# Performance work log

Hardware: AMD Instinct MI355X
Metric: run time of the kernel (lower is better)

Reference implementation:

```python
import jax, jax.numpy as jnp
import numpy as np

INPUT_SIZE = 512
HIDDEN_SIZE = 1024
SEQ_LEN = 512
BATCH = 64


def _xavier(key, shape):
    fan_out, fan_in = shape
    limit = float(np.sqrt(6.0 / (fan_in + fan_out)))
    return jax.random.uniform(key, shape, jnp.float32, -limit, limit)


def setup_inputs() -> dict:
    key = jax.random.key(0)
    ks = jax.random.split(key, 10)
    return {
        "x_seq": jax.random.normal(ks[0], (SEQ_LEN, BATCH, INPUT_SIZE), jnp.float32),
        "h": jax.random.normal(ks[1], (BATCH, HIDDEN_SIZE), jnp.float32),
        "U_c": _xavier(ks[2], (HIDDEN_SIZE, INPUT_SIZE)),
        "w_c": jax.random.normal(ks[3], (HIDDEN_SIZE,), jnp.float32),
        "b_c": jax.random.normal(ks[4], (HIDDEN_SIZE,), jnp.float32),
        "U_a": _xavier(ks[5], (HIDDEN_SIZE, INPUT_SIZE)),
        "w_a": jax.random.normal(ks[6], (HIDDEN_SIZE,), jnp.float32),
        "b_a": jax.random.normal(ks[7], (HIDDEN_SIZE,), jnp.float32),
        "U_h": _xavier(ks[8], (HIDDEN_SIZE, INPUT_SIZE)),
        "b_h": jax.random.normal(ks[9], (HIDDEN_SIZE,), jnp.float32),
    }


def reference(x_seq, h, U_c, w_c, b_c, U_a, w_a, b_a, U_h, b_h):
    # Precompute all input projections in one big batched GEMM each:
    # (S, B, I) @ (I, H) -> (S, B, H)
    xc = jnp.einsum("sbi,hi->sbh", x_seq, U_c) + b_c
    xa = jnp.einsum("sbi,hi->sbh", x_seq, U_a) + b_a
    xh = jnp.einsum("sbi,hi->sbh", x_seq, U_h) + b_h

    def step(h, proj):
        pc, pa, ph = proj
        c = jax.nn.sigmoid(pc + w_c * h)
        a = 1.0 + jnp.tanh(pa + w_a * h)
        h_new = c * h + (1.0 - c) * jnp.tanh(ph + a * h)
        return h_new, h_new

    hn, y_seq = jax.lax.scan(step, h, (xc, xa, xh))
    return y_seq, hn
```

## Files before the change

kernel.cpp:

```cpp
#include <hip/hip_runtime.h>
#include <hip/hip_bf16.h>
#include <stdint.h>

#define SEQLEN 512
#define NBATCH 64
#define KDIM   512
#define HDIM   1024
#define MTOT   (SEQLEN * NBATCH)
#define NTOT   (3 * HDIM)
#define STRIDE (NBATCH * HDIM)

typedef __attribute__((ext_vector_type(4)))  float f32x4;
typedef __attribute__((ext_vector_type(16))) float f32x16;
typedef _Float16 f16x8 __attribute__((ext_vector_type(8)));

__global__ __launch_bounds__(256) void cvt_x(const float* __restrict__ x,
                                             _Float16* __restrict__ xh,
                                             _Float16* __restrict__ xl) {
    int i = blockIdx.x * 256 + threadIdx.x;
    const float4* s = (const float4*)(x + (size_t)i * 8);
    float4 a = s[0], b = s[1];
    float v[8] = {a.x, a.y, a.z, a.w, b.x, b.y, b.z, b.w};
    f16x8 hi, lo;
#pragma unroll
    for (int j = 0; j < 8; ++j) {
        _Float16 h = (_Float16)v[j];
        hi[j] = h;
        lo[j] = (_Float16)(v[j] - (float)h);
    }
    *(f16x8*)(xh + (size_t)i * 8) = hi;
    *(f16x8*)(xl + (size_t)i * 8) = lo;
}

__global__ __launch_bounds__(256) void cvt_u(const float* __restrict__ Uc,
                                             const float* __restrict__ Ua,
                                             const float* __restrict__ Uh,
                                             _Float16* __restrict__ uh,
                                             _Float16* __restrict__ ul) {
    int i = blockIdx.x * 256 + threadIdx.x;
    int n = i >> 6;
    int kb = (i & 63) * 8;
    const float* src = (n < HDIM) ? (Uc + (size_t)n * KDIM)
                     : (n < 2 * HDIM) ? (Ua + (size_t)(n - HDIM) * KDIM)
                     : (Uh + (size_t)(n - 2 * HDIM) * KDIM);
    const float4* s = (const float4*)(src + kb);
    float4 a = s[0], b = s[1];
    float v[8] = {a.x, a.y, a.z, a.w, b.x, b.y, b.z, b.w};
    f16x8 hi, lo;
#pragma unroll
    for (int j = 0; j < 8; ++j) {
        _Float16 h = (_Float16)v[j];
        hi[j] = h;
        lo[j] = (_Float16)(v[j] - (float)h);
    }
    *(f16x8*)(uh + (size_t)n * KDIM + kb) = hi;
    *(f16x8*)(ul + (size_t)n * KDIM + kb) = lo;
}

#define BM 256
#define BN 256
#define BK 32
#define NT_N (NTOT / BN)
#define GRID ((MTOT / BM) * NT_N)
#define KT_N (KDIM / BK)

__device__ __forceinline__ void gload16(const _Float16* g, _Float16* l) {
    __builtin_amdgcn_global_load_lds((const __attribute__((address_space(1))) void*)g,
                                     (__attribute__((address_space(3))) void*)l,
                                     16, 0, 0);
}

__device__ __forceinline__ f32x16 mfma32(f16x8 a, f16x8 b, f32x16 c) {
    return __builtin_amdgcn_mfma_f32_32x32x16_f16(a, b, c, 0, 0, 0);
}

__global__ __launch_bounds__(512, 2) void gemm_f16x2(const _Float16* __restrict__ Ah,
                                                     const _Float16* __restrict__ Al,
                                                     const _Float16* __restrict__ Bh,
                                                     const _Float16* __restrict__ Bl,
                                                     float* __restrict__ pc,
                                                     float* __restrict__ pa,
                                                     float* __restrict__ ph) {
    __shared__ _Float16 lds[2][4][BM * BK];

    int bid  = blockIdx.x;
    int bm   = bid / NT_N;
    int bn   = bid % NT_N;
    int tid  = threadIdx.x;
    int lane = tid & 63;
    int wave = tid >> 6;
    int wr   = wave >> 2;
    int wc   = wave & 3;

    size_t row_off = (size_t)(tid >> 2) * KDIM
                   + (size_t)(((tid & 3) ^ ((tid >> 3) & 3)) * 8);
    const _Float16* gAh = Ah + (size_t)bm * BM * KDIM + row_off;
    const _Float16* gAl = Al + (size_t)bm * BM * KDIM + row_off;
    const _Float16* gBh = Bh + (size_t)bn * BN * KDIM + row_off;
    const _Float16* gBl = Bl + (size_t)bn * BN * KDIM + row_off;
    const size_t HPAN = (size_t)128 * KDIM;
    int t8 = tid * 8;

#define SPAIR(buf, plane, gp, kt) do { int _g = (kt) * BK;                     \
    gload16((gp) + _g,        &lds[buf][plane][t8]);                           \
    gload16((gp) + HPAN + _g, &lds[buf][plane][t8 + 4096]); } while (0)

    f32x16 acc[4][2];
#pragma unroll
    for (int i = 0; i < 4; ++i)
#pragma unroll
        for (int j = 0; j < 2; ++j)
#pragma unroll
            for (int r = 0; r < 16; ++r)
                acc[i][j][r] = 0.f;

    int rr = lane & 31;
    int kg = lane >> 5;
    int kx = (lane >> 1) & 3;

    f16x8 a_[4][2], b_[2][2];

#define READ_A(ks) _Pragma("unroll")                                           \
    for (int i = 0; i < 4; ++i) {                                              \
        int row = wr * 128 + i * 32 + rr;                                      \
        int ko = ((((ks) * 2 + kg) ^ kx) * 8);                                 \
        a_[i][0] = *(const f16x8*)(&lds[cur][0][row * BK + ko]);               \
        a_[i][1] = *(const f16x8*)(&lds[cur][1][row * BK + ko]);               \
    }
#define READ_B(ks) _Pragma("unroll")                                           \
    for (int j = 0; j < 2; ++j) {                                              \
        int row = wc * 64 + j * 32 + rr;                                       \
        int ko = ((((ks) * 2 + kg) ^ kx) * 8);                                 \
        b_[j][0] = *(const f16x8*)(&lds[cur][2][row * BK + ko]);               \
        b_[j][1] = *(const f16x8*)(&lds[cur][3][row * BK + ko]);               \
    }
#define MFMA_STEP() _Pragma("unroll")                                          \
    for (int i = 0; i < 4; ++i) _Pragma("unroll")                              \
        for (int j = 0; j < 2; ++j) {                                          \
            f32x16 c = acc[i][j];                                              \
            c = mfma32(a_[i][0], b_[j][1], c);                      \
            c = mfma32(a_[i][1], b_[j][0], c);                      \
            c = mfma32(a_[i][0], b_[j][0], c);                      \
            acc[i][j] = c;                                                     \
        }

    SPAIR(0, 0, gAh, 0); SPAIR(0, 1, gAl, 0);
    SPAIR(0, 2, gBh, 0); SPAIR(0, 3, gBl, 0);

    for (int kt = 0; kt < KT_N; ++kt) {
        int cur = kt & 1, nxt = 1 - cur;
        bool pre = (kt < KT_N - 1);
        __builtin_amdgcn_sched_barrier(0);
        asm volatile("s_waitcnt vmcnt(0)" ::: "memory");
        __builtin_amdgcn_s_barrier();
        __builtin_amdgcn_sched_barrier(0);

        READ_B(0);
        READ_A(0);
        if (pre) { SPAIR(nxt, 0, gAh, kt + 1); SPAIR(nxt, 1, gAl, kt + 1); }
        __builtin_amdgcn_s_setprio(1);
        MFMA_STEP();
        __builtin_amdgcn_s_setprio(0);
        READ_A(1);
        READ_B(1);
        if (pre) { SPAIR(nxt, 2, gBh, kt + 1); SPAIR(nxt, 3, gBl, kt + 1); }
        __builtin_amdgcn_s_setprio(1);
        MFMA_STEP();
        __builtin_amdgcn_s_setprio(0);
    }

    int n0 = bn * BN;
    float* outp; int nb;
    if (n0 < HDIM)            { outp = pc; nb = n0; }
    else if (n0 < 2 * HDIM)   { outp = pa; nb = n0 - HDIM; }
    else                      { outp = ph; nb = n0 - 2 * HDIM; }

#pragma unroll
    for (int i = 0; i < 4; ++i)
#pragma unroll
        for (int j = 0; j < 2; ++j) {
            int mbase = bm * BM + wr * 128 + i * 32 + 4 * kg;
            int nn = nb + wc * 64 + j * 32 + rr;
#pragma unroll
            for (int t = 0; t < 4; ++t)
#pragma unroll
                for (int q = 0; q < 4; ++q)
                    outp[(size_t)(mbase + q + 8 * t) * HDIM + nn] = acc[i][j][t * 4 + q];
        }
#undef SPAIR
#undef READ_A
#undef READ_B
#undef MFMA_STEP
}

__device__ __forceinline__ float fsigmoid(float z) {
    float e = __expf(-z);
    return __builtin_amdgcn_rcpf(1.0f + e);
}
__device__ __forceinline__ float ftanh(float x) {
    float ax = fminf(fabsf(x), 10.0f);
    float e  = __expf(-2.0f * ax);
    float t  = (1.0f - e) * __builtin_amdgcn_rcpf(1.0f + e);
    return copysignf(t, x);
}

__global__ __launch_bounds__(256) void recur(const float* __restrict__ pc_a,
                                             const float* __restrict__ pa_a,
                                             float* out,
                                             const float* __restrict__ h0,
                                             const float* __restrict__ wc_,
                                             const float* __restrict__ bc_,
                                             const float* __restrict__ wa_,
                                             const float* __restrict__ ba_,
                                             const float* __restrict__ bh_) {
    int idx = blockIdx.x * 256 + threadIdx.x;
    int j = idx & (HDIM - 1);
    float h  = h0[idx];
    float wc = wc_[j], bc = bc_[j];
    float wa = wa_[j], ba = ba_[j];
    float bh = bh_[j];

#define PF 32
    float pc[PF], pa[PF], ph[PF];
#pragma unroll
    for (int u = 0; u < PF; ++u) {
        pc[u] = pc_a[(size_t)u * STRIDE + idx];
        pa[u] = pa_a[(size_t)u * STRIDE + idx];
        ph[u] = out [(size_t)u * STRIDE + idx];
    }

    for (int sb = 0; sb < SEQLEN; sb += PF) {
#pragma unroll
        for (int u = 0; u < PF; ++u) {
            int s = sb + u;
            float vc = pc[u], va = pa[u], vh = ph[u];
            int sp = s + PF; sp = (sp < SEQLEN) ? sp : (SEQLEN - 1);
            pc[u] = pc_a[(size_t)sp * STRIDE + idx];
            pa[u] = pa_a[(size_t)sp * STRIDE + idx];
            ph[u] = out [(size_t)sp * STRIDE + idx];

            float zc = (vc + bc) + wc * h;
            float za = (va + ba) + wa * h;
            float c  = fsigmoid(zc);
            float a  = 1.0f + ftanh(za);
            float ht = ftanh((vh + bh) + a * h);
            h = c * h + (1.0f - c) * ht;
            out[(size_t)s * STRIDE + idx] = h;
        }
    }
    out[(size_t)SEQLEN * STRIDE + idx] = h;
}

extern "C" void kernel_launch(void* const* d_in, const int* in_sizes, int n_in,
                              void* d_out, int out_size, void* d_ws, size_t ws_size,
                              hipStream_t stream) {
    const float* x_seq = (const float*)d_in[0];
    const float* h0    = (const float*)d_in[1];
    const float* U_c   = (const float*)d_in[2];
    const float* w_c   = (const float*)d_in[3];
    const float* b_c   = (const float*)d_in[4];
    const float* U_a   = (const float*)d_in[5];
    const float* w_a   = (const float*)d_in[6];
    const float* b_a   = (const float*)d_in[7];
    const float* U_h   = (const float*)d_in[8];
    const float* b_h   = (const float*)d_in[9];
    float* out = (float*)d_out;

    char* ws = (char*)d_ws;
    const size_t MB = 1024 * 1024;
    float*    ws_pc = (float*)ws;
    float*    ws_pa = (float*)(ws + 128 * MB);
    _Float16* x_hi  = (_Float16*)(ws + 256 * MB);
    _Float16* x_lo  = (_Float16*)(ws + 288 * MB);
    _Float16* u_hi  = (_Float16*)(ws + 320 * MB);
    _Float16* u_lo  = (_Float16*)(ws + 323 * MB);

    cvt_x<<<dim3(MTOT * KDIM / 8 / 256), dim3(256), 0, stream>>>(x_seq, x_hi, x_lo);
    cvt_u<<<dim3(NTOT * KDIM / 8 / 256), dim3(256), 0, stream>>>(U_c, U_a, U_h, u_hi, u_lo);
    gemm_f16x2<<<dim3(GRID), dim3(512), 0, stream>>>(
        x_hi, x_lo, u_hi, u_lo, ws_pc, ws_pa, out);
    recur<<<dim3(STRIDE / 256), dim3(256), 0, stream>>>(ws_pc, ws_pa, out, h0,
                                                        w_c, b_c, w_a, b_a, b_h);
}
```

Before: 494.2 us.

## Merge conversion kernels, deepen LDS swizzle, shrink recurrence prefetch, use libm activations

```diff
diff --git a/kernel.cpp b/kernel.cpp
--- a/kernel.cpp
+++ b/kernel.cpp
@@ -14,11 +14,35 @@
 typedef __attribute__((ext_vector_type(16))) float f32x16;
 typedef _Float16 f16x8 __attribute__((ext_vector_type(8)));
 
-__global__ __launch_bounds__(256) void cvt_x(const float* __restrict__ x,
-                                             _Float16* __restrict__ xh,
-                                             _Float16* __restrict__ xl) {
+#define XTHREADS (MTOT * KDIM / 8)
+#define UTHREADS (NTOT * KDIM / 8)
+__global__ __launch_bounds__(256) void cvt_all(const float* __restrict__ x,
+                                               const float* __restrict__ Uc,
+                                               const float* __restrict__ Ua,
+                                               const float* __restrict__ Uh,
+                                               _Float16* __restrict__ xh,
+                                               _Float16* __restrict__ xl,
+                                               _Float16* __restrict__ uh,
+                                               _Float16* __restrict__ ul) {
     int i = blockIdx.x * 256 + threadIdx.x;
-    const float4* s = (const float4*)(x + (size_t)i * 8);
+    const float* src;
+    _Float16 *dh, *dl;
+    size_t off;
+    if (i < XTHREADS) {
+        src = x + (size_t)i * 8;
+        off = (size_t)i * 8;
+        dh = xh; dl = xl;
+    } else {
+        int u = i - XTHREADS;
+        int n = u >> 6;
+        int kb = (u & 63) * 8;
+        src = ((n < HDIM) ? (Uc + (size_t)n * KDIM)
+             : (n < 2 * HDIM) ? (Ua + (size_t)(n - HDIM) * KDIM)
+             : (Uh + (size_t)(n - 2 * HDIM) * KDIM)) + kb;
+        off = (size_t)n * KDIM + kb;
+        dh = uh; dl = ul;
+    }
+    const float4* s = (const float4*)src;
     float4 a = s[0], b = s[1];
     float v[8] = {a.x, a.y, a.z, a.w, b.x, b.y, b.z, b.w};
     f16x8 hi, lo;
@@ -28,33 +52,8 @@
         hi[j] = h;
         lo[j] = (_Float16)(v[j] - (float)h);
     }
-    *(f16x8*)(xh + (size_t)i * 8) = hi;
-    *(f16x8*)(xl + (size_t)i * 8) = lo;
-}
-
-__global__ __launch_bounds__(256) void cvt_u(const float* __restrict__ Uc,
-                                             const float* __restrict__ Ua,
-                                             const float* __restrict__ Uh,
-                                             _Float16* __restrict__ uh,
-                                             _Float16* __restrict__ ul) {
-    int i = blockIdx.x * 256 + threadIdx.x;
-    int n = i >> 6;
-    int kb = (i & 63) * 8;
-    const float* src = (n < HDIM) ? (Uc + (size_t)n * KDIM)
-                     : (n < 2 * HDIM) ? (Ua + (size_t)(n - HDIM) * KDIM)
-                     : (Uh + (size_t)(n - 2 * HDIM) * KDIM);
-    const float4* s = (const float4*)(src + kb);
-    float4 a = s[0], b = s[1];
-    float v[8] = {a.x, a.y, a.z, a.w, b.x, b.y, b.z, b.w};
-    f16x8 hi, lo;
-#pragma unroll
-    for (int j = 0; j < 8; ++j) {
-        _Float16 h = (_Float16)v[j];
-        hi[j] = h;
-        lo[j] = (_Float16)(v[j] - (float)h);
-    }
-    *(f16x8*)(uh + (size_t)n * KDIM + kb) = hi;
-    *(f16x8*)(ul + (size_t)n * KDIM + kb) = lo;
+    *(f16x8*)(dh + off) = hi;
+    *(f16x8*)(dl + off) = lo;
 }
 
 #define BM 256
@@ -93,17 +92,17 @@
     int wc   = wave & 3;
 
     size_t row_off = (size_t)(tid >> 2) * KDIM
-                   + (size_t)(((tid & 3) ^ ((tid >> 3) & 3)) * 8);
+        + (size_t)((((tid & 3) ^ ((tid >> 3) & 3) ^ ((tid >> 5) & 3))) * 8);
     const _Float16* gAh = Ah + (size_t)bm * BM * KDIM + row_off;
     const _Float16* gAl = Al + (size_t)bm * BM * KDIM + row_off;
     const _Float16* gBh = Bh + (size_t)bn * BN * KDIM + row_off;
     const _Float16* gBl = Bl + (size_t)bn * BN * KDIM + row_off;
-    const size_t HPAN = (size_t)128 * KDIM;
+    const size_t P128 = (size_t)128 * KDIM;
     int t8 = tid * 8;
 
 #define SPAIR(buf, plane, gp, kt) do { int _g = (kt) * BK;                     \
     gload16((gp) + _g,        &lds[buf][plane][t8]);                           \
-    gload16((gp) + HPAN + _g, &lds[buf][plane][t8 + 4096]); } while (0)
+    gload16((gp) + P128 + _g, &lds[buf][plane][t8 + 4096]); } while (0)
 
     f32x16 acc[4][2];
 #pragma unroll
@@ -116,21 +115,21 @@
 
     int rr = lane & 31;
     int kg = lane >> 5;
-    int kx = (lane >> 1) & 3;
+    int q12 = ((lane >> 1) & 3) ^ ((lane >> 3) & 3);
 
     f16x8 a_[4][2], b_[2][2];
 
 #define READ_A(ks) _Pragma("unroll")                                           \
     for (int i = 0; i < 4; ++i) {                                              \
         int row = wr * 128 + i * 32 + rr;                                      \
-        int ko = ((((ks) * 2 + kg) ^ kx) * 8);                                 \
+        int ko = ((((ks) * 2 + kg) ^ q12) * 8);                                \
         a_[i][0] = *(const f16x8*)(&lds[cur][0][row * BK + ko]);               \
         a_[i][1] = *(const f16x8*)(&lds[cur][1][row * BK + ko]);               \
     }
 #define READ_B(ks) _Pragma("unroll")                                           \
     for (int j = 0; j < 2; ++j) {                                              \
         int row = wc * 64 + j * 32 + rr;                                       \
-        int ko = ((((ks) * 2 + kg) ^ kx) * 8);                                 \
+        int ko = ((((ks) * 2 + kg) ^ q12) * 8);                                \
         b_[j][0] = *(const f16x8*)(&lds[cur][2][row * BK + ko]);               \
         b_[j][1] = *(const f16x8*)(&lds[cur][3][row * BK + ko]);               \
     }
@@ -191,17 +190,6 @@
 #undef READ_A
 #undef READ_B
 #undef MFMA_STEP
-}
-
-__device__ __forceinline__ float fsigmoid(float z) {
-    float e = __expf(-z);
-    return __builtin_amdgcn_rcpf(1.0f + e);
-}
-__device__ __forceinline__ float ftanh(float x) {
-    float ax = fminf(fabsf(x), 10.0f);
-    float e  = __expf(-2.0f * ax);
-    float t  = (1.0f - e) * __builtin_amdgcn_rcpf(1.0f + e);
-    return copysignf(t, x);
 }
 
 __global__ __launch_bounds__(256) void recur(const float* __restrict__ pc_a,
@@ -220,7 +208,7 @@
     float wa = wa_[j], ba = ba_[j];
     float bh = bh_[j];
 
-#define PF 32
+#define PF 16
     float pc[PF], pa[PF], ph[PF];
 #pragma unroll
     for (int u = 0; u < PF; ++u) {
@@ -241,9 +229,9 @@
 
             float zc = (vc + bc) + wc * h;
             float za = (va + ba) + wa * h;
-            float c  = fsigmoid(zc);
-            float a  = 1.0f + ftanh(za);
-            float ht = ftanh((vh + bh) + a * h);
+            float c  = 1.0f / (1.0f + expf(-zc));
+            float a  = 1.0f + tanhf(za);
+            float ht = tanhf((vh + bh) + a * h);
             h = c * h + (1.0f - c) * ht;
             out[(size_t)s * STRIDE + idx] = h;
         }
@@ -275,8 +263,8 @@
     _Float16* u_hi  = (_Float16*)(ws + 320 * MB);
     _Float16* u_lo  = (_Float16*)(ws + 323 * MB);
 
-    cvt_x<<<dim3(MTOT * KDIM / 8 / 256), dim3(256), 0, stream>>>(x_seq, x_hi, x_lo);
-    cvt_u<<<dim3(NTOT * KDIM / 8 / 256), dim3(256), 0, stream>>>(U_c, U_a, U_h, u_hi, u_lo);
+    cvt_all<<<dim3((XTHREADS + UTHREADS) / 256), dim3(256), 0, stream>>>(
+        x_seq, U_c, U_a, U_h, x_hi, x_lo, u_hi, u_lo);
     gemm_f16x2<<<dim3(GRID), dim3(512), 0, stream>>>(
         x_hi, x_lo, u_hi, u_lo, ws_pc, ws_pa, out);
     recur<<<dim3(STRIDE / 256), dim3(256), 0, stream>>>(ws_pc, ws_pa, out, h0,
```

After: 493.7 us. Within noise of the previous version (-0.1%).
